# Kernel tuning notes

Measured on AMD Instinct MI355X. Metric: run time of the kernel, lower is better.

## Reference

```python
import jax, jax.numpy as jnp
import numpy as np


def setup_inputs() -> dict:
    key = jax.random.key(0)
    kb, kc = jax.random.split(key)
    B, P, N, D = 64, 8192, 128, 2
    batch = jax.random.uniform(kb, (B, P, D), dtype=jnp.float32)
    not_dummy = jnp.ones((B, P), dtype=jnp.float32)  # all points valid
    centers = jax.random.uniform(kc, (N, D), dtype=jnp.float32)
    sharpness = jnp.ones((N, D), dtype=jnp.float32) * 3.0  # default init: ones * 3
    return {"batch": batch, "not_dummy": not_dummy, "centers": centers, "sharpness": sharpness}


def reference(batch, not_dummy, centers, sharpness):
    # batch: [B, P, d]; not_dummy: [B, P]; centers/sharpness: [N, d]
    # RBF kernel per (batch, element, point): exp(-sum_d sharpness*(center-point)^2)
    diff = centers[None, :, None, :] - batch[:, None, :, :]          # [B, N, P, d]
    dist = jnp.sum(diff * diff * sharpness[None, :, None, :], axis=-1)  # [B, N, P]
    x = jnp.exp(-dist) * not_dummy[:, None, :]                        # mask dummy points
    out = jnp.sum(x, axis=-1)                                         # [B, N]
    return jnp.squeeze(out)
```

## Files before the change

kernel.cpp:

```cpp
#include <hip/hip_runtime.h>

typedef float v2f __attribute__((ext_vector_type(2)));

#define NTILE 8
#define NPAIR (NTILE / 2)
#define THREADS 256

static __device__ __forceinline__ v2f pk_fma(v2f a, v2f b, v2f c) {
    v2f d;
    asm("v_pk_fma_f32 %0, %1, %2, %3" : "=v"(d) : "v"(a), "v"(b), "v"(c));
    return d;
}
static __device__ __forceinline__ v2f pk_mul(v2f a, v2f b) {
    v2f d;
    asm("v_pk_mul_f32 %0, %1, %2" : "=v"(d) : "v"(a), "v"(b));
    return d;
}

static __device__ __forceinline__ v2f fast_exp_pair(v2f u) {
    v2f r;
    r.x = __int_as_float((int)u.x);
    r.y = __int_as_float((int)u.y);
    return r;
}

template <bool R2>
static __device__ __forceinline__ void point_body(
    float x0, float x1, float mk,
    const v2f* Av, const v2f* Bv, const v2f* Cv, const v2f* Dv, const v2f* Ev,
    v2f* acc)
{
    const v2f sx0 = {x0, x0};
    const v2f sx1 = {x1, x1};
    const v2f smk = {mk, mk};
    if (R2) {
        const float r2 = __builtin_fmaf(x1, x1, x0 * x0);
        const v2f sr2 = {r2, r2};
#pragma unroll
        for (int i = 0; i < NPAIR; ++i) {
            v2f t = pk_fma(Dv[i], sr2, Av[i]);
            t = pk_fma(Bv[i], sx0, t);
            t = pk_fma(Cv[i], sx1, t);
            acc[i] = pk_fma(fast_exp_pair(t), smk, acc[i]);
        }
    } else {
        const v2f sq0 = pk_mul(sx0, sx0);
        const v2f sq1 = pk_mul(sx1, sx1);
#pragma unroll
        for (int i = 0; i < NPAIR; ++i) {
            v2f t = pk_fma(Bv[i], sx0, Av[i]);
            t = pk_fma(Cv[i], sx1, t);
            t = pk_fma(Dv[i], sq0, t);
            t = pk_fma(Ev[i], sq1, t);
            acc[i] = pk_fma(fast_exp_pair(t), smk, acc[i]);
        }
    }
}

template <bool R2>
static __device__ __forceinline__ void main_loop(
    const float4* B4, const float4* M4, int quads, int tid,
    const v2f* Av, const v2f* Bv, const v2f* Cv, const v2f* Dv, const v2f* Ev,
    v2f* acc)
{
    int q = tid;
    if (q >= quads) return;
    float4 pa = B4[2 * q], pb = B4[2 * q + 1], pm = M4[q];
    while (true) {
        const int qn = q + THREADS;
        const bool vn = qn < quads;
        const int qc = vn ? qn : q;
        float4 na = B4[2 * qc], nb = B4[2 * qc + 1], nm = M4[qc];

        point_body<R2>(pa.x, pa.y, pm.x, Av, Bv, Cv, Dv, Ev, acc);
        point_body<R2>(pa.z, pa.w, pm.y, Av, Bv, Cv, Dv, Ev, acc);
        point_body<R2>(pb.x, pb.y, pm.z, Av, Bv, Cv, Dv, Ev, acc);
        point_body<R2>(pb.z, pb.w, pm.w, Av, Bv, Cv, Dv, Ev, acc);

        if (!vn) break;
        q = qn; pa = na; pb = nb; pm = nm;
    }
}

__global__ __launch_bounds__(THREADS, 4) void slayer_exp_kernel(
    const float* __restrict__ batch,
    const float* __restrict__ not_dummy,
    const float* __restrict__ centers,
    const float* __restrict__ sharpness,
    float* __restrict__ out,
    int B, int P, int N, int T)
{
    const int id = blockIdx.x;
    int b, j;
    if ((B & 7) == 0) {
        const int r = id >> 3;
        j = r % T;
        b = (r / T) * 8 + (id & 7);
    } else {
        b = id / T;
        j = id % T;
    }
    const int n0  = j * NTILE;
    const int tid = threadIdx.x;

    const float S    = 12102203.161561485f;
    const float BIAS = 1064872549.0f;

    v2f Av[NPAIR], Bv[NPAIR], Cv[NPAIR], Dv[NPAIR], Ev[NPAIR];
    bool iso = true;
#pragma unroll
    for (int i = 0; i < NPAIR; ++i) {
#pragma unroll
        for (int h = 0; h < 2; ++h) {
            int n = n0 + 2 * i + h;
            if (n >= N) n = N - 1;
            float c0 = centers[2 * n + 0];
            float c1 = centers[2 * n + 1];
            float s0 = sharpness[2 * n + 0];
            float s1 = sharpness[2 * n + 1];
            Av[i][h] = BIAS - S * (s0 * c0 * c0 + s1 * c1 * c1);
            Bv[i][h] = S * 2.0f * s0 * c0;
            Cv[i][h] = S * 2.0f * s1 * c1;
            Dv[i][h] = -S * s0;
            Ev[i][h] = -S * s1;
            iso = iso && (s0 == s1);
        }
    }

    v2f acc[NPAIR];
#pragma unroll
    for (int i = 0; i < NPAIR; ++i) acc[i] = (v2f){0.0f, 0.0f};

    const float4* B4 = (const float4*)(batch + (size_t)b * P * 2);
    const float4* M4 = (const float4*)(not_dummy + (size_t)b * P);
    const int quads = P >> 2;

    if (iso) main_loop<true>(B4, M4, quads, tid, Av, Bv, Cv, Dv, Ev, acc);
    else     main_loop<false>(B4, M4, quads, tid, Av, Bv, Cv, Dv, Ev, acc);

    if ((P & 3) && tid == 0) {
        const float* bb = batch + (size_t)b * P * 2;
        const float* mm = not_dummy + (size_t)b * P;
        for (int p = (quads << 2); p < P; ++p)
            point_body<false>(bb[2 * p], bb[2 * p + 1], mm[p], Av, Bv, Cv, Dv, Ev, acc);
    }

    float red8[NTILE];
#pragma unroll
    for (int i = 0; i < NPAIR; ++i) { red8[2 * i] = acc[i].x; red8[2 * i + 1] = acc[i].y; }
#pragma unroll
    for (int i = 0; i < NTILE; ++i) {
        float v = red8[i];
#pragma unroll
        for (int off = 32; off >= 1; off >>= 1)
            v += __shfl_xor(v, off, 64);
        red8[i] = v;
    }

    __shared__ float red[THREADS / 64][NTILE];
    const int wave = tid >> 6;
    const int lane = tid & 63;
    if (lane == 0) {
#pragma unroll
        for (int i = 0; i < NTILE; ++i) red[wave][i] = red8[i];
    }
    __syncthreads();

    if (tid < NTILE && (n0 + tid) < N) {
        float v = 0.0f;
#pragma unroll
        for (int w = 0; w < THREADS / 64; ++w) v += red[w][tid];
        out[(size_t)b * N + n0 + tid] = v;
    }
}

extern "C" void kernel_launch(void* const* d_in, const int* in_sizes, int n_in,
                              void* d_out, int out_size, void* d_ws, size_t ws_size,
                              hipStream_t stream) {
    const float* batch     = (const float*)d_in[0];
    const float* not_dummy = (const float*)d_in[1];
    const float* centers   = (const float*)d_in[2];
    const float* sharp     = (const float*)d_in[3];
    float* out = (float*)d_out;

    const int N  = in_sizes[2] / 2;
    const int BP = in_sizes[1];
    const int B  = out_size / N;
    const int P  = BP / B;
    const int T  = (N + NTILE - 1) / NTILE;

    dim3 grid(T * B);
    slayer_exp_kernel<<<grid, THREADS, 0, stream>>>(batch, not_dummy, centers, sharp,
                                                    out, B, P, N, T);
}
```

Before: 16.94 us.

## Widen center tile to 16 and block to 512 threads, split anisotropic path

Doubles the number of centers each block handles and the threads per block, so each loaded point is reused across 16 centers and the grid shrinks by half. The isotropic path keeps all 16 centers' coefficients in registers. The anisotropic path runs two passes of 8 centers to limit register pressure. The tail handler now computes directly from centers instead of using precomputed coefficients. Risks include higher register use and fewer blocks (512 instead of 1024), which may hurt occupancy and load balance; launch_bounds(THREADS,4) with 512 threads may also force register spilling.

```diff
diff --git a/kernel.cpp b/kernel.cpp
--- a/kernel.cpp
+++ b/kernel.cpp
@@ -2,9 +2,10 @@
 
 typedef float v2f __attribute__((ext_vector_type(2)));
 
-#define NTILE 8
-#define NPAIR (NTILE / 2)
-#define THREADS 256
+#define THREADS 512
+#define NTILE 16
+#define NPAIR 8
+#define NPAIR2 4
 
 static __device__ __forceinline__ v2f pk_fma(v2f a, v2f b, v2f c) {
     v2f d;
@@ -24,40 +25,44 @@
     return r;
 }
 
-template <bool R2>
-static __device__ __forceinline__ void point_body(
+#define S_CONST    12102203.161561485f
+#define BIAS_CONST 1064872549.0f
+
+template <int NP>
+static __device__ __forceinline__ void body_iso(
+    float x0, float x1, float mk,
+    const v2f* Av, const v2f* Bv, const v2f* Cv, const v2f* Dv, v2f* acc)
+{
+    const float r2 = __builtin_fmaf(x1, x1, x0 * x0);
+    const v2f sr2 = {r2, r2}, sx0 = {x0, x0}, sx1 = {x1, x1}, smk = {mk, mk};
+#pragma unroll
+    for (int i = 0; i < NP; ++i) {
+        v2f t = pk_fma(Dv[i], sr2, Av[i]);
+        t = pk_fma(Bv[i], sx0, t);
+        t = pk_fma(Cv[i], sx1, t);
+        acc[i] = pk_fma(fast_exp_pair(t), smk, acc[i]);
+    }
+}
+
+template <int NP>
+static __device__ __forceinline__ void body_gen(
     float x0, float x1, float mk,
     const v2f* Av, const v2f* Bv, const v2f* Cv, const v2f* Dv, const v2f* Ev,
     v2f* acc)
 {
-    const v2f sx0 = {x0, x0};
-    const v2f sx1 = {x1, x1};
-    const v2f smk = {mk, mk};
-    if (R2) {
-        const float r2 = __builtin_fmaf(x1, x1, x0 * x0);
-        const v2f sr2 = {r2, r2};
-#pragma unroll
-        for (int i = 0; i < NPAIR; ++i) {
-            v2f t = pk_fma(Dv[i], sr2, Av[i]);
-            t = pk_fma(Bv[i], sx0, t);
-            t = pk_fma(Cv[i], sx1, t);
-            acc[i] = pk_fma(fast_exp_pair(t), smk, acc[i]);
-        }
-    } else {
-        const v2f sq0 = pk_mul(sx0, sx0);
-        const v2f sq1 = pk_mul(sx1, sx1);
-#pragma unroll
-        for (int i = 0; i < NPAIR; ++i) {
-            v2f t = pk_fma(Bv[i], sx0, Av[i]);
-            t = pk_fma(Cv[i], sx1, t);
-            t = pk_fma(Dv[i], sq0, t);
-            t = pk_fma(Ev[i], sq1, t);
-            acc[i] = pk_fma(fast_exp_pair(t), smk, acc[i]);
-        }
-    }
-}
-
-template <bool R2>
+    const v2f sx0 = {x0, x0}, sx1 = {x1, x1}, smk = {mk, mk};
+    const v2f sq0 = pk_mul(sx0, sx0), sq1 = pk_mul(sx1, sx1);
+#pragma unroll
+    for (int i = 0; i < NP; ++i) {
+        v2f t = pk_fma(Bv[i], sx0, Av[i]);
+        t = pk_fma(Cv[i], sx1, t);
+        t = pk_fma(Dv[i], sq0, t);
+        t = pk_fma(Ev[i], sq1, t);
+        acc[i] = pk_fma(fast_exp_pair(t), smk, acc[i]);
+    }
+}
+
+template <int NP, bool ISO>
 static __device__ __forceinline__ void main_loop(
     const float4* B4, const float4* M4, int quads, int tid,
     const v2f* Av, const v2f* Bv, const v2f* Cv, const v2f* Dv, const v2f* Ev,
@@ -72,10 +77,17 @@
         const int qc = vn ? qn : q;
         float4 na = B4[2 * qc], nb = B4[2 * qc + 1], nm = M4[qc];
 
-        point_body<R2>(pa.x, pa.y, pm.x, Av, Bv, Cv, Dv, Ev, acc);
-        point_body<R2>(pa.z, pa.w, pm.y, Av, Bv, Cv, Dv, Ev, acc);
-        point_body<R2>(pb.x, pb.y, pm.z, Av, Bv, Cv, Dv, Ev, acc);
-        point_body<R2>(pb.z, pb.w, pm.w, Av, Bv, Cv, Dv, Ev, acc);
+        if (ISO) {
+            body_iso<NP>(pa.x, pa.y, pm.x, Av, Bv, Cv, Dv, acc);
+            body_iso<NP>(pa.z, pa.w, pm.y, Av, Bv, Cv, Dv, acc);
+            body_iso<NP>(pb.x, pb.y, pm.z, Av, Bv, Cv, Dv, acc);
+            body_iso<NP>(pb.z, pb.w, pm.w, Av, Bv, Cv, Dv, acc);
+        } else {
+            body_gen<NP>(pa.x, pa.y, pm.x, Av, Bv, Cv, Dv, Ev, acc);
+            body_gen<NP>(pa.z, pa.w, pm.y, Av, Bv, Cv, Dv, Ev, acc);
+            body_gen<NP>(pb.x, pb.y, pm.z, Av, Bv, Cv, Dv, Ev, acc);
+            body_gen<NP>(pb.z, pb.w, pm.w, Av, Bv, Cv, Dv, Ev, acc);
+        }
 
         if (!vn) break;
         q = qn; pa = na; pb = nb; pm = nm;
@@ -103,28 +115,11 @@
     const int n0  = j * NTILE;
     const int tid = threadIdx.x;
 
-    const float S    = 12102203.161561485f;
-    const float BIAS = 1064872549.0f;
-
-    v2f Av[NPAIR], Bv[NPAIR], Cv[NPAIR], Dv[NPAIR], Ev[NPAIR];
     bool iso = true;
 #pragma unroll
-    for (int i = 0; i < NPAIR; ++i) {
-#pragma unroll
-        for (int h = 0; h < 2; ++h) {
-            int n = n0 + 2 * i + h;
-            if (n >= N) n = N - 1;
-            float c0 = centers[2 * n + 0];
-            float c1 = centers[2 * n + 1];
-            float s0 = sharpness[2 * n + 0];
-            float s1 = sharpness[2 * n + 1];
-            Av[i][h] = BIAS - S * (s0 * c0 * c0 + s1 * c1 * c1);
-            Bv[i][h] = S * 2.0f * s0 * c0;
-            Cv[i][h] = S * 2.0f * s1 * c1;
-            Dv[i][h] = -S * s0;
-            Ev[i][h] = -S * s1;
-            iso = iso && (s0 == s1);
-        }
+    for (int i = 0; i < NTILE; ++i) {
+        int n = n0 + i; if (n >= N) n = N - 1;
+        iso = iso && (sharpness[2 * n] == sharpness[2 * n + 1]);
     }
 
     v2f acc[NPAIR];
@@ -135,26 +130,71 @@
     const float4* M4 = (const float4*)(not_dummy + (size_t)b * P);
     const int quads = P >> 2;
 
-    if (iso) main_loop<true>(B4, M4, quads, tid, Av, Bv, Cv, Dv, Ev, acc);
-    else     main_loop<false>(B4, M4, quads, tid, Av, Bv, Cv, Dv, Ev, acc);
+    if (iso) {
+        v2f Av[NPAIR], Bv[NPAIR], Cv[NPAIR], Dv[NPAIR];
+#pragma unroll
+        for (int i = 0; i < NPAIR; ++i) {
+#pragma unroll
+            for (int h = 0; h < 2; ++h) {
+                int n = n0 + 2 * i + h; if (n >= N) n = N - 1;
+                float c0 = centers[2 * n], c1 = centers[2 * n + 1];
+                float s0 = sharpness[2 * n], s1 = sharpness[2 * n + 1];
+                Av[i][h] = BIAS_CONST - S_CONST * (s0 * c0 * c0 + s1 * c1 * c1);
+                Bv[i][h] = S_CONST * 2.0f * s0 * c0;
+                Cv[i][h] = S_CONST * 2.0f * s1 * c1;
+                Dv[i][h] = -S_CONST * s0;
+            }
+        }
+        main_loop<NPAIR, true>(B4, M4, quads, tid, Av, Bv, Cv, Dv, nullptr, acc);
+    } else {
+        for (int pass = 0; pass < 2; ++pass) {
+            v2f Av[NPAIR2], Bv[NPAIR2], Cv[NPAIR2], Dv[NPAIR2], Ev[NPAIR2];
+#pragma unroll
+            for (int i = 0; i < NPAIR2; ++i) {
+#pragma unroll
+                for (int h = 0; h < 2; ++h) {
+                    int n = n0 + (pass * NPAIR2 + i) * 2 + h; if (n >= N) n = N - 1;
+                    float c0 = centers[2 * n], c1 = centers[2 * n + 1];
+                    float s0 = sharpness[2 * n], s1 = sharpness[2 * n + 1];
+                    Av[i][h] = BIAS_CONST - S_CONST * (s0 * c0 * c0 + s1 * c1 * c1);
+                    Bv[i][h] = S_CONST * 2.0f * s0 * c0;
+                    Cv[i][h] = S_CONST * 2.0f * s1 * c1;
+                    Dv[i][h] = -S_CONST * s0;
+                    Ev[i][h] = -S_CONST * s1;
+                }
+            }
+            main_loop<NPAIR2, false>(B4, M4, quads, tid, Av, Bv, Cv, Dv, Ev,
+                                     acc + pass * NPAIR2);
+        }
+    }
 
     if ((P & 3) && tid == 0) {
         const float* bb = batch + (size_t)b * P * 2;
         const float* mm = not_dummy + (size_t)b * P;
-        for (int p = (quads << 2); p < P; ++p)
-            point_body<false>(bb[2 * p], bb[2 * p + 1], mm[p], Av, Bv, Cv, Dv, Ev, acc);
-    }
-
-    float red8[NTILE];
-#pragma unroll
-    for (int i = 0; i < NPAIR; ++i) { red8[2 * i] = acc[i].x; red8[2 * i + 1] = acc[i].y; }
+        for (int p = (quads << 2); p < P; ++p) {
+            float x0 = bb[2 * p], x1 = bb[2 * p + 1], m = mm[p];
+#pragma unroll
+            for (int i = 0; i < NTILE; ++i) {
+                int n = n0 + i; if (n >= N) n = N - 1;
+                float c0 = centers[2 * n], c1 = centers[2 * n + 1];
+                float s0 = sharpness[2 * n], s1 = sharpness[2 * n + 1];
+                float d0 = x0 - c0, d1 = x1 - c1;
+                float u = BIAS_CONST - S_CONST * (s0 * d0 * d0 + s1 * d1 * d1);
+                acc[i >> 1][i & 1] += __int_as_float((int)u) * m;
+            }
+        }
+    }
+
+    float red16[NTILE];
+#pragma unroll
+    for (int i = 0; i < NPAIR; ++i) { red16[2 * i] = acc[i].x; red16[2 * i + 1] = acc[i].y; }
 #pragma unroll
     for (int i = 0; i < NTILE; ++i) {
-        float v = red8[i];
+        float v = red16[i];
 #pragma unroll
         for (int off = 32; off >= 1; off >>= 1)
             v += __shfl_xor(v, off, 64);
-        red8[i] = v;
+        red16[i] = v;
     }
 
     __shared__ float red[THREADS / 64][NTILE];
@@ -162,7 +202,7 @@
     const int lane = tid & 63;
     if (lane == 0) {
 #pragma unroll
-        for (int i = 0; i < NTILE; ++i) red[wave][i] = red8[i];
+        for (int i = 0; i < NTILE; ++i) red[wave][i] = red16[i];
     }
     __syncthreads();
 
```

Result: slower. 17.46 us (+3.1%).

## Replace packed FMA with scalar FMAs using SGPR-uniform coefficients, 512 threads

Applied to the files above, without the earlier changes.

Drops the v_pk_fma_f32 inline asm in favour of scalar fmaf loops, with the per-center coefficients forced into scalar registers via readfirstlane so they take no VGPRs. The block size doubles to 512 threads and the launch-bounds occupancy hint goes from 4 to 8. The aim is to free vector registers and raise occupancy, and to let one operand of each FMA come from an SGPR. The cost is twice as many VALU instructions as the packed path, and each block now streams its points with twice as many threads.

```diff
diff --git a/kernel.cpp b/kernel.cpp
--- a/kernel.cpp
+++ b/kernel.cpp
@@ -1,67 +1,51 @@
 #include <hip/hip_runtime.h>
 
-typedef float v2f __attribute__((ext_vector_type(2)));
+#define THREADS 512
+#define NTILE 8
 
-#define NTILE 8
-#define NPAIR (NTILE / 2)
-#define THREADS 256
+#define S_CONST    12102203.161561485f
+#define BIAS_CONST 1064872549.0f
 
-static __device__ __forceinline__ v2f pk_fma(v2f a, v2f b, v2f c) {
-    v2f d;
-    asm("v_pk_fma_f32 %0, %1, %2, %3" : "=v"(d) : "v"(a), "v"(b), "v"(c));
-    return d;
-}
-static __device__ __forceinline__ v2f pk_mul(v2f a, v2f b) {
-    v2f d;
-    asm("v_pk_mul_f32 %0, %1, %2" : "=v"(d) : "v"(a), "v"(b));
-    return d;
+static __device__ __forceinline__ float uni(float x) {
+    return __int_as_float(__builtin_amdgcn_readfirstlane(__float_as_int(x)));
 }
 
-static __device__ __forceinline__ v2f fast_exp_pair(v2f u) {
-    v2f r;
-    r.x = __int_as_float((int)u.x);
-    r.y = __int_as_float((int)u.y);
-    return r;
-}
-
-template <bool R2>
-static __device__ __forceinline__ void point_body(
+static __device__ __forceinline__ void body_iso(
     float x0, float x1, float mk,
-    const v2f* Av, const v2f* Bv, const v2f* Cv, const v2f* Dv, const v2f* Ev,
-    v2f* acc)
+    const float* cA, const float* cB, const float* cC, const float* cD,
+    float* acc)
 {
-    const v2f sx0 = {x0, x0};
-    const v2f sx1 = {x1, x1};
-    const v2f smk = {mk, mk};
-    if (R2) {
-        const float r2 = __builtin_fmaf(x1, x1, x0 * x0);
-        const v2f sr2 = {r2, r2};
+    const float r2 = __builtin_fmaf(x1, x1, x0 * x0);
 #pragma unroll
-        for (int i = 0; i < NPAIR; ++i) {
-            v2f t = pk_fma(Dv[i], sr2, Av[i]);
-            t = pk_fma(Bv[i], sx0, t);
-            t = pk_fma(Cv[i], sx1, t);
-            acc[i] = pk_fma(fast_exp_pair(t), smk, acc[i]);
-        }
-    } else {
-        const v2f sq0 = pk_mul(sx0, sx0);
-        const v2f sq1 = pk_mul(sx1, sx1);
-#pragma unroll
-        for (int i = 0; i < NPAIR; ++i) {
-            v2f t = pk_fma(Bv[i], sx0, Av[i]);
-            t = pk_fma(Cv[i], sx1, t);
-            t = pk_fma(Dv[i], sq0, t);
-            t = pk_fma(Ev[i], sq1, t);
-            acc[i] = pk_fma(fast_exp_pair(t), smk, acc[i]);
-        }
+    for (int i = 0; i < NTILE; ++i) {
+        float t = __builtin_fmaf(cD[i], r2, cA[i]);
+        t = __builtin_fmaf(cB[i], x0, t);
+        t = __builtin_fmaf(cC[i], x1, t);
+        acc[i] = __builtin_fmaf(__int_as_float((int)t), mk, acc[i]);
     }
 }
 
-template <bool R2>
+static __device__ __forceinline__ void body_gen(
+    float x0, float x1, float mk,
+    const float* cA, const float* cB, const float* cC, const float* cD,
+    const float* cE, float* acc)
+{
+    const float sq0 = x0 * x0, sq1 = x1 * x1;
+#pragma unroll
+    for (int i = 0; i < NTILE; ++i) {
+        float t = __builtin_fmaf(cB[i], x0, cA[i]);
+        t = __builtin_fmaf(cC[i], x1, t);
+        t = __builtin_fmaf(cD[i], sq0, t);
+        t = __builtin_fmaf(cE[i], sq1, t);
+        acc[i] = __builtin_fmaf(__int_as_float((int)t), mk, acc[i]);
+    }
+}
+
+template <bool ISO>
 static __device__ __forceinline__ void main_loop(
     const float4* B4, const float4* M4, int quads, int tid,
-    const v2f* Av, const v2f* Bv, const v2f* Cv, const v2f* Dv, const v2f* Ev,
-    v2f* acc)
+    const float* cA, const float* cB, const float* cC, const float* cD,
+    const float* cE, float* acc)
 {
     int q = tid;
     if (q >= quads) return;
@@ -72,17 +56,24 @@
         const int qc = vn ? qn : q;
         float4 na = B4[2 * qc], nb = B4[2 * qc + 1], nm = M4[qc];
 
-        point_body<R2>(pa.x, pa.y, pm.x, Av, Bv, Cv, Dv, Ev, acc);
-        point_body<R2>(pa.z, pa.w, pm.y, Av, Bv, Cv, Dv, Ev, acc);
-        point_body<R2>(pb.x, pb.y, pm.z, Av, Bv, Cv, Dv, Ev, acc);
-        point_body<R2>(pb.z, pb.w, pm.w, Av, Bv, Cv, Dv, Ev, acc);
+        if (ISO) {
+            body_iso(pa.x, pa.y, pm.x, cA, cB, cC, cD, acc);
+            body_iso(pa.z, pa.w, pm.y, cA, cB, cC, cD, acc);
+            body_iso(pb.x, pb.y, pm.z, cA, cB, cC, cD, acc);
+            body_iso(pb.z, pb.w, pm.w, cA, cB, cC, cD, acc);
+        } else {
+            body_gen(pa.x, pa.y, pm.x, cA, cB, cC, cD, cE, acc);
+            body_gen(pa.z, pa.w, pm.y, cA, cB, cC, cD, cE, acc);
+            body_gen(pb.x, pb.y, pm.z, cA, cB, cC, cD, cE, acc);
+            body_gen(pb.z, pb.w, pm.w, cA, cB, cC, cD, cE, acc);
+        }
 
         if (!vn) break;
         q = qn; pa = na; pb = nb; pm = nm;
     }
 }
 
-__global__ __launch_bounds__(THREADS, 4) void slayer_exp_kernel(
+__global__ __launch_bounds__(THREADS, 8) void slayer_exp_kernel(
     const float* __restrict__ batch,
     const float* __restrict__ not_dummy,
     const float* __restrict__ centers,
@@ -103,58 +94,46 @@
     const int n0  = j * NTILE;
     const int tid = threadIdx.x;
 
-    const float S    = 12102203.161561485f;
-    const float BIAS = 1064872549.0f;
-
-    v2f Av[NPAIR], Bv[NPAIR], Cv[NPAIR], Dv[NPAIR], Ev[NPAIR];
+    float cA[NTILE], cB[NTILE], cC[NTILE], cD[NTILE], cE[NTILE];
     bool iso = true;
 #pragma unroll
-    for (int i = 0; i < NPAIR; ++i) {
-#pragma unroll
-        for (int h = 0; h < 2; ++h) {
-            int n = n0 + 2 * i + h;
-            if (n >= N) n = N - 1;
-            float c0 = centers[2 * n + 0];
-            float c1 = centers[2 * n + 1];
-            float s0 = sharpness[2 * n + 0];
-            float s1 = sharpness[2 * n + 1];
-            Av[i][h] = BIAS - S * (s0 * c0 * c0 + s1 * c1 * c1);
-            Bv[i][h] = S * 2.0f * s0 * c0;
-            Cv[i][h] = S * 2.0f * s1 * c1;
-            Dv[i][h] = -S * s0;
-            Ev[i][h] = -S * s1;
-            iso = iso && (s0 == s1);
-        }
+    for (int i = 0; i < NTILE; ++i) {
+        int n = n0 + i; if (n >= N) n = N - 1;
+        const float c0 = centers[2 * n], c1 = centers[2 * n + 1];
+        const float s0 = sharpness[2 * n], s1 = sharpness[2 * n + 1];
+        cA[i] = BIAS_CONST - S_CONST * (s0 * c0 * c0 + s1 * c1 * c1);
+        cB[i] = uni(S_CONST * 2.0f * s0 * c0);
+        cC[i] = uni(S_CONST * 2.0f * s1 * c1);
+        cD[i] = uni(-S_CONST * s0);
+        cE[i] = uni(-S_CONST * s1);
+        iso = iso && (s0 == s1);
     }
 
-    v2f acc[NPAIR];
+    float acc[NTILE];
 #pragma unroll
-    for (int i = 0; i < NPAIR; ++i) acc[i] = (v2f){0.0f, 0.0f};
+    for (int i = 0; i < NTILE; ++i) acc[i] = 0.0f;
 
     const float4* B4 = (const float4*)(batch + (size_t)b * P * 2);
     const float4* M4 = (const float4*)(not_dummy + (size_t)b * P);
     const int quads = P >> 2;
 
-    if (iso) main_loop<true>(B4, M4, quads, tid, Av, Bv, Cv, Dv, Ev, acc);
-    else     main_loop<false>(B4, M4, quads, tid, Av, Bv, Cv, Dv, Ev, acc);
+    if (iso) main_loop<true>(B4, M4, quads, tid, cA, cB, cC, cD, cE, acc);
+    else     main_loop<false>(B4, M4, quads, tid, cA, cB, cC, cD, cE, acc);
 
     if ((P & 3) && tid == 0) {
         const float* bb = batch + (size_t)b * P * 2;
         const float* mm = not_dummy + (size_t)b * P;
         for (int p = (quads << 2); p < P; ++p)
-            point_body<false>(bb[2 * p], bb[2 * p + 1], mm[p], Av, Bv, Cv, Dv, Ev, acc);
+            body_gen(bb[2 * p], bb[2 * p + 1], mm[p], cA, cB, cC, cD, cE, acc);
     }
 
-    float red8[NTILE];
-#pragma unroll
-    for (int i = 0; i < NPAIR; ++i) { red8[2 * i] = acc[i].x; red8[2 * i + 1] = acc[i].y; }
 #pragma unroll
     for (int i = 0; i < NTILE; ++i) {
-        float v = red8[i];
+        float v = acc[i];
 #pragma unroll
         for (int off = 32; off >= 1; off >>= 1)
             v += __shfl_xor(v, off, 64);
-        red8[i] = v;
+        acc[i] = v;
     }
 
     __shared__ float red[THREADS / 64][NTILE];
@@ -162,7 +141,7 @@
     const int lane = tid & 63;
     if (lane == 0) {
 #pragma unroll
-        for (int i = 0; i < NTILE; ++i) red[wave][i] = red8[i];
+        for (int i = 0; i < NTILE; ++i) red[wave][i] = acc[i];
     }
     __syncthreads();
 
```

Measured after the change: 17.88 us. 1.06x slower.
